# Performance work log

Hardware: AMD Instinct MI355X
Metric: run time of the kernel (lower is better)

The kernel has to match this reference:

```python
import jax, jax.numpy as jnp
import numpy as np

NEG = -1e30  # log-space 'minus infinity' that stays finite in fp32 arithmetic
BLANK = 0


def _lse3(a, b, c):
    m = jnp.maximum(jnp.maximum(a, b), c)
    return m + jnp.log(jnp.exp(a - m) + jnp.exp(b - m) + jnp.exp(c - m))


def setup_inputs() -> dict:
    key = jax.random.key(0)
    k1, k2, k3, k4 = jax.random.split(key, 4)
    B, T, C, L = 16, 512, 4096, 128
    scores = jax.random.normal(k1, (B, T, C), dtype=jnp.float32)
    labels = jax.random.randint(k2, (B, L), 1, C, dtype=jnp.int64)      # no blanks in targets
    feat_lens = jax.random.randint(k3, (B,), 384, T + 1, dtype=jnp.int64)
    label_lens = jax.random.randint(k4, (B,), 64, L + 1, dtype=jnp.int64)
    return {"scores": scores, "labels": labels, "feat_lens": feat_lens, "label_lens": label_lens}


def reference(scores, labels, feat_lens, label_lens):
    # scores: [B, T, C]. Matches torch: log_softmax then nn.CTCLoss(blank=0,
    # reduction='mean', zero_infinity=True).
    scores = scores.astype(jnp.float32)
    log_probs = jax.nn.log_softmax(scores, axis=-1)                      # [B, T, C]
    B, T, C = scores.shape
    L = labels.shape[1]
    S = 2 * L + 1  # extended label: blank, l1, blank, ..., lL, blank

    ext = jnp.full((B, S), BLANK, dtype=labels.dtype).at[:, 1::2].set(labels)
    # Gather per-(t, extended-symbol) log-probs once: [B, T, S]
    lp = jnp.take_along_axis(log_probs, jnp.broadcast_to(ext[:, None, :], (B, T, S)), axis=2)

    # skip transition s-2 -> s allowed iff ext[s] != blank and ext[s] != ext[s-2]
    skip = jnp.concatenate(
        [jnp.zeros((B, 2), bool), (ext[:, 2:] != ext[:, :-2]) & (ext[:, 2:] != BLANK)], axis=1)

    alpha0 = jnp.full((B, S), NEG, dtype=jnp.float32).at[:, 0].set(lp[:, 0, 0])
    alpha0 = alpha0.at[:, 1].set(jnp.where(label_lens > 0, lp[:, 0, 1], NEG))

    lp_t_first = jnp.swapaxes(lp, 0, 1)  # [T, B, S]

    def step(alpha, xs):
        lp_t, t = xs
        a1 = jnp.pad(alpha, ((0, 0), (1, 0)), constant_values=NEG)[:, :S]
        a2 = jnp.pad(alpha, ((0, 0), (2, 0)), constant_values=NEG)[:, :S]
        a2 = jnp.where(skip, a2, NEG)
        new = lp_t + _lse3(alpha, a1, a2)
        alpha = jnp.where((t < feat_lens)[:, None], new, alpha)  # freeze past feat_len
        return alpha, None

    alpha, _ = jax.lax.scan(step, alpha0, (lp_t_first[1:], jnp.arange(1, T)))

    end = 2 * label_lens  # index of final blank per sample
    a_end = jnp.take_along_axis(alpha, end[:, None], axis=1)[:, 0]
    a_end1 = jnp.where(
        label_lens > 0,
        jnp.take_along_axis(alpha, jnp.maximum(end - 1, 0)[:, None], axis=1)[:, 0], NEG)
    m = jnp.maximum(a_end, a_end1)
    log_lik = m + jnp.log(jnp.exp(a_end - m) + jnp.exp(a_end1 - m))
    loss = -log_lik
    loss = jnp.where(loss > 0.5e30, 0.0, loss)  # zero_infinity=True
    denom = jnp.maximum(label_lens, 1).astype(loss.dtype)
    return jnp.mean(loss / denom)  # torch 'mean': divide by target_lengths, then batch mean
```

## Files before the change

### kernel.cpp

```cpp
#include <hip/hip_runtime.h>

#define T_ 512
#define C_ 4096
#define L_ 128
#define NEGF (-1e30f)
#define RCPLN2 1.4426950408889634f
#define LN2 0.6931471805599453f

__device__ __forceinline__ float fexp2(float x) { return __builtin_amdgcn_exp2f(x); }
__device__ __forceinline__ float flog2(float x) { return __builtin_amdgcn_logf(x); }

__device__ __forceinline__ float lse2_2(float a, float b) {
  float m = fmaxf(a, b);
  float d = a - b;
  return m + flog2(1.0f + fexp2(-fabsf(d)));
}
__device__ __forceinline__ float lse3_2(float a, float b, float c) {
  float m = fmaxf(fmaxf(a, b), c);
  return m + flog2(fexp2(a - m) + fexp2(b - m) + fexp2(c - m));
}

__global__ __launch_bounds__(256) void k_lse_gather(
    const float* __restrict__ scores, const int* __restrict__ labels,
    const int* __restrict__ feat_lens,
    float* __restrict__ lp_lab, float* __restrict__ lp_blank) {
  const int row = blockIdx.x;
  const int b = row >> 9;
  const int t = row & (T_ - 1);
  if (t >= feat_lens[b]) return;

  __shared__ float sRow[C_];
  __shared__ float sSum[4];
  const float4* __restrict__ rp4 = (const float4*)(scores + (size_t)row * C_);
  float4* sRow4 = (float4*)sRow;
  const int tid = threadIdx.x;

  float s0 = 0.f, s1 = 0.f, s2 = 0.f, s3 = 0.f;
#pragma unroll
  for (int k = 0; k < 4; ++k) {
    float4 v = rp4[tid + 256 * k];
    sRow4[tid + 256 * k] = v;
    s0 += fexp2(v.x * RCPLN2);
    s1 += fexp2(v.y * RCPLN2);
    s2 += fexp2(v.z * RCPLN2);
    s3 += fexp2(v.w * RCPLN2);
  }
  float s = (s0 + s1) + (s2 + s3);
#pragma unroll
  for (int off = 32; off; off >>= 1) s += __shfl_down(s, off);
  const int wid = tid >> 6, lane = tid & 63;
  if (lane == 0) sSum[wid] = s;
  __syncthreads();
  const float l2sum = flog2((sSum[0] + sSum[1]) + (sSum[2] + sSum[3]));

  if (tid < L_) {
    const int lab = labels[b * L_ + tid];
    lp_lab[(size_t)row * L_ + tid] = sRow[lab] * RCPLN2 - l2sum;
  } else if (tid == L_) {
    lp_blank[row] = sRow[0] * RCPLN2 - l2sum;
  }
}

__global__ __launch_bounds__(128) void k_ctc_dp(
    const float* __restrict__ lp_lab, const float* __restrict__ lp_blank,
    const int* __restrict__ labels, const int* __restrict__ feat_lens,
    const int* __restrict__ label_lens, float* __restrict__ loss_out) {
  const int b = blockIdx.x;
  const int lane = threadIdx.x & 63;
  const int wid = threadIdx.x >> 6;
  const int flen = feat_lens[b];
  const int llen = label_lens[b];
  const int tm = flen >> 1;

  const int l0 = labels[b * L_ + 2 * lane];
  const int l1 = labels[b * L_ + 2 * lane + 1];
  const int lm1 = __shfl_up(l1, 1);
  const int ln0 = __shfl_down(l0, 1);
  const bool skip1 = (lane > 0) && (l0 != lm1);
  const bool skip3 = (l1 != l0);
  const bool skipd = (lane < 63) && (ln0 != l1);

  const float2* __restrict__ llp = (const float2*)(lp_lab + (size_t)b * T_ * L_);
  const float* __restrict__ lpl = lp_lab + (size_t)b * T_ * L_;
  const float* __restrict__ lbp = lp_blank + b * T_;

  __shared__ float sB[257];

  if (wid == 0) {
    const float2 ll0 = llp[lane];
    float a0 = (lane == 0) ? lbp[0] : NEGF;
    float a1 = (lane == 0) ? ll0.x : NEGF;
    float a2 = NEGF, a3 = NEGF, a4 = NEGF;
    float p = NEGF;

    float2 cc[4]; float cb[4];
#pragma unroll
    for (int k = 0; k < 4; ++k) {
      const int tt = min(1 + k, flen - 1);
      cc[k] = llp[tt * 64 + lane]; cb[k] = lbp[tt];
    }
    int t = 1;
    while (t <= tm) {
      float2 nc[4]; float nb[4];
#pragma unroll
      for (int k = 0; k < 4; ++k) {
        const int tt = min(t + 4 + k, flen - 1);
        nc[k] = llp[tt * 64 + lane]; nb[k] = lbp[tt];
      }
#pragma unroll
      for (int k = 0; k < 4; ++k) {
        if (t + k <= tm) {
          const float n3 = cc[k].y + lse3_2(a3, a2, skip3 ? a1 : NEGF);
          const float n4 = cb[k] + lse2_2(a4, a3);
          const float pn = __shfl_up(n3, 1);
          const float n0 = cb[k] + lse2_2(a0, p);
          const float n1 = cc[k].x + lse3_2(a1, a0, skip1 ? p : NEGF);
          const float n2 = cb[k] + lse2_2(a2, a1);
          a0 = n0; a1 = n1; a2 = n2; a3 = n3; a4 = n4;
          p = (lane == 0) ? NEGF : pn;
        }
      }
#pragma unroll
      for (int k = 0; k < 4; ++k) { cc[k] = nc[k]; cb[k] = nb[k]; }
      t += 4;
    }
    const float2 cce = llp[tm * 64 + lane];
    const float cbe = lbp[tm];
    const float c0 = a0 - cbe, c1 = a1 - cce.x, c2 = a2 - cbe, c3 = a3 - cce.y;
    const float c4 = a4 - cbe;
    __syncthreads();
    float v0 = c0 + sB[4 * lane + 0];
    float v1 = c1 + sB[4 * lane + 1];
    float v2 = c2 + sB[4 * lane + 2];
    float v3 = c3 + sB[4 * lane + 3];
    float m = fmaxf(fmaxf(v0, v1), fmaxf(v2, v3));
    float v4 = NEGF;
    if (lane == 63) { v4 = c4 + sB[256]; m = fmaxf(m, v4); }
#pragma unroll
    for (int off = 1; off < 64; off <<= 1) m = fmaxf(m, __shfl_xor(m, off));
    float sum = fexp2(v0 - m) + fexp2(v1 - m) + fexp2(v2 - m) + fexp2(v3 - m);
    if (lane == 63) sum += fexp2(v4 - m);
#pragma unroll
    for (int off = 1; off < 64; off <<= 1) sum += __shfl_xor(sum, off);
    if (lane == 0) {
      const float l2lik = m + flog2(sum);
      float loss = -LN2 * l2lik;
      if (loss > 0.5e30f) loss = 0.0f;
      loss_out[b] = loss / (float)llen;
    }
  } else {
    const int e = 2 * llen;
    const float ve = lbp[flen - 1];
    const float vo = lpl[(size_t)(flen - 1) * L_ + (llen - 1)];
    float b0 = (4 * lane == e) ? ve : NEGF;
    float b1 = (4 * lane + 1 == e - 1) ? vo : NEGF;
    float b2 = (4 * lane + 2 == e) ? ve : NEGF;
    float b3 = (4 * lane + 3 == e - 1) ? vo : NEGF;
    float b4 = (lane == 63 && e == 256) ? ve : NEGF;
    float q0 = __shfl_down(b0, 1); q0 = (lane == 63) ? b4 : q0;
    float q1 = __shfl_down(b1, 1); q1 = (lane == 63) ? NEGF : q1;

    float2 cc[4]; float cb[4];
    int t = flen - 2;
#pragma unroll
    for (int k = 0; k < 4; ++k) {
      const int tt = max(t - k, tm);
      cc[k] = llp[tt * 64 + lane]; cb[k] = lbp[tt];
    }
    while (t >= tm) {
      float2 nc[4]; float nb[4];
#pragma unroll
      for (int k = 0; k < 4; ++k) {
        const int tt = max(t - 4 - k, tm);
        nc[k] = llp[tt * 64 + lane]; nb[k] = lbp[tt];
      }
#pragma unroll
      for (int k = 0; k < 4; ++k) {
        if (t - k >= tm) {
          const float n0 = cb[k] + lse2_2(b0, b1);
          const float n1 = cc[k].x + lse3_2(b1, b2, skip3 ? b3 : NEGF);
          const float n4 = cb[k] + b4;
          const float q0n = __shfl_down(n0, 1);
          const float q1n = __shfl_down(n1, 1);
          const float n3 = cc[k].y + lse3_2(b3, q0, skipd ? q1 : NEGF);
          const float n2 = cb[k] + lse2_2(b2, b3);
          b0 = n0; b1 = n1; b2 = n2; b3 = n3; b4 = n4;
          q0 = (lane == 63) ? n4 : q0n;
          q1 = (lane == 63) ? NEGF : q1n;
        }
      }
#pragma unroll
      for (int k = 0; k < 4; ++k) { cc[k] = nc[k]; cb[k] = nb[k]; }
      t -= 4;
    }
    sB[4 * lane + 0] = b0;
    sB[4 * lane + 1] = b1;
    sB[4 * lane + 2] = b2;
    sB[4 * lane + 3] = b3;
    if (lane == 63) sB[256] = b4;
    __syncthreads();
  }
}

__global__ __launch_bounds__(64) void k_final(const float* __restrict__ loss_out,
                                              float* __restrict__ out, int B) {
  const int tid = threadIdx.x;
  float v = (tid < B) ? loss_out[tid] : 0.0f;
#pragma unroll
  for (int off = 32; off; off >>= 1) v += __shfl_down(v, off);
  if (tid == 0) out[0] = v / (float)B;
}

extern "C" void kernel_launch(void* const* d_in, const int* in_sizes, int n_in,
                              void* d_out, int out_size, void* d_ws, size_t ws_size,
                              hipStream_t stream) {
  const float* scores = (const float*)d_in[0];
  const int* labels = (const int*)d_in[1];
  const int* feat_lens = (const int*)d_in[2];
  const int* label_lens = (const int*)d_in[3];
  const int B = in_sizes[2];

  float* lp_lab = (float*)d_ws;
  float* lp_blank = lp_lab + (size_t)B * T_ * L_;
  float* loss_out = lp_blank + (size_t)B * T_;
  float* out = (float*)d_out;

  k_lse_gather<<<B * T_, 256, 0, stream>>>(scores, labels, feat_lens, lp_lab, lp_blank);
  k_ctc_dp<<<B, 128, 0, stream>>>(lp_lab, lp_blank, labels, feat_lens, label_lens, loss_out);
  k_final<<<1, 64, 0, stream>>>(loss_out, out, B);
}
```

Measured before the change: 231.8 us.

## Run CTC forward-backward recursion in scaled probability space instead of log space

The log-softmax gather now emits probabilities (exp2 of the log-prob), and the alpha/beta recursions switch from log-sum-exp to plain multiply-adds. Every two steps a wave-wide max rescales the state, and the log of that scale is accumulated so underflow is avoided. This removes the per-step exp/log transcendental chain on the serial DP critical path. In exchange it adds a wave-wide max reduction and a reciprocal every two steps, and precision changes, for example probabilities underflowing in fp32 when a single step's probabilities are very small.

Result: slower. 243.7 us (+5.1%).

```diff
diff --git a/kernel.cpp b/kernel.cpp
--- a/kernel.cpp
+++ b/kernel.cpp
@@ -3,27 +3,21 @@
 #define T_ 512
 #define C_ 4096
 #define L_ 128
-#define NEGF (-1e30f)
 #define RCPLN2 1.4426950408889634f
 #define LN2 0.6931471805599453f
+#define NEGL (-1e30f)
+#define SCALE_CTR 4.722366482869645e21f
+#define SCALE_LOG 72.0f
 
 __device__ __forceinline__ float fexp2(float x) { return __builtin_amdgcn_exp2f(x); }
 __device__ __forceinline__ float flog2(float x) { return __builtin_amdgcn_logf(x); }
-
-__device__ __forceinline__ float lse2_2(float a, float b) {
-  float m = fmaxf(a, b);
-  float d = a - b;
-  return m + flog2(1.0f + fexp2(-fabsf(d)));
-}
-__device__ __forceinline__ float lse3_2(float a, float b, float c) {
-  float m = fmaxf(fmaxf(a, b), c);
-  return m + flog2(fexp2(a - m) + fexp2(b - m) + fexp2(c - m));
-}
+__device__ __forceinline__ float frcp(float x)  { return __builtin_amdgcn_rcpf(x); }
+__device__ __forceinline__ float lg(float x)    { return (x > 0.f) ? flog2(x) : NEGL; }
 
 __global__ __launch_bounds__(256) void k_lse_gather(
     const float* __restrict__ scores, const int* __restrict__ labels,
     const int* __restrict__ feat_lens,
-    float* __restrict__ lp_lab, float* __restrict__ lp_blank) {
+    float* __restrict__ p_lab, float* __restrict__ p_blank) {
   const int row = blockIdx.x;
   const int b = row >> 9;
   const int t = row & (T_ - 1);
@@ -55,14 +49,14 @@
 
   if (tid < L_) {
     const int lab = labels[b * L_ + tid];
-    lp_lab[(size_t)row * L_ + tid] = sRow[lab] * RCPLN2 - l2sum;
+    p_lab[(size_t)row * L_ + tid] = fexp2(sRow[lab] * RCPLN2 - l2sum);
   } else if (tid == L_) {
-    lp_blank[row] = sRow[0] * RCPLN2 - l2sum;
+    p_blank[row] = fexp2(sRow[0] * RCPLN2 - l2sum);
   }
 }
 
 __global__ __launch_bounds__(128) void k_ctc_dp(
-    const float* __restrict__ lp_lab, const float* __restrict__ lp_blank,
+    const float* __restrict__ p_lab, const float* __restrict__ p_blank,
     const int* __restrict__ labels, const int* __restrict__ feat_lens,
     const int* __restrict__ label_lens, float* __restrict__ loss_out) {
   const int b = blockIdx.x;
@@ -80,18 +74,20 @@
   const bool skip3 = (l1 != l0);
   const bool skipd = (lane < 63) && (ln0 != l1);
 
-  const float2* __restrict__ llp = (const float2*)(lp_lab + (size_t)b * T_ * L_);
-  const float* __restrict__ lpl = lp_lab + (size_t)b * T_ * L_;
-  const float* __restrict__ lbp = lp_blank + b * T_;
+  const float2* __restrict__ llp = (const float2*)(p_lab + (size_t)b * T_ * L_);
+  const float* __restrict__ lpl = p_lab + (size_t)b * T_ * L_;
+  const float* __restrict__ lbp = p_blank + b * T_;
 
   __shared__ float sB[257];
+  __shared__ float sSb;
 
   if (wid == 0) {
     const float2 ll0 = llp[lane];
-    float a0 = (lane == 0) ? lbp[0] : NEGF;
-    float a1 = (lane == 0) ? ll0.x : NEGF;
-    float a2 = NEGF, a3 = NEGF, a4 = NEGF;
-    float p = NEGF;
+    float a0 = (lane == 0) ? lbp[0] : 0.f;
+    float a1 = (lane == 0) ? ll0.x : 0.f;
+    float a2 = 0.f, a3 = 0.f, a4 = 0.f;
+    float p = 0.f;
+    float Sa = 0.f;
 
     float2 cc[4]; float cb[4];
 #pragma unroll
@@ -110,14 +106,23 @@
 #pragma unroll
       for (int k = 0; k < 4; ++k) {
         if (t + k <= tm) {
-          const float n3 = cc[k].y + lse3_2(a3, a2, skip3 ? a1 : NEGF);
-          const float n4 = cb[k] + lse2_2(a4, a3);
+          const float n3 = cc[k].y * (a3 + a2 + (skip3 ? a1 : 0.f));
+          const float n4 = cb[k] * (a4 + a3);
           const float pn = __shfl_up(n3, 1);
-          const float n0 = cb[k] + lse2_2(a0, p);
-          const float n1 = cc[k].x + lse3_2(a1, a0, skip1 ? p : NEGF);
-          const float n2 = cb[k] + lse2_2(a2, a1);
-          a0 = n0; a1 = n1; a2 = n2; a3 = n3; a4 = n4;
-          p = (lane == 0) ? NEGF : pn;
+          const float n0 = cb[k] * (a0 + p);
+          const float n1 = cc[k].x * (a1 + a0 + (skip1 ? p : 0.f));
+          const float n2 = cb[k] * (a2 + a1);
+          a0 = n0; a1 = n1; a2 = n2; a3 = n3;
+          a4 = (lane == 63) ? n4 : 0.f;
+          p = (lane == 0) ? 0.f : pn;
+        }
+        if (k & 1) {
+          float m = fmaxf(fmaxf(fmaxf(a0, a1), fmaxf(a2, a3)), a4);
+#pragma unroll
+          for (int off = 1; off < 64; off <<= 1) m = fmaxf(m, __shfl_xor(m, off));
+          const float r = frcp(m) * SCALE_CTR;
+          Sa += flog2(m) - SCALE_LOG;
+          a0 *= r; a1 *= r; a2 *= r; a3 *= r; a4 *= r; p *= r;
         }
       }
 #pragma unroll
@@ -126,39 +131,41 @@
     }
     const float2 cce = llp[tm * 64 + lane];
     const float cbe = lbp[tm];
-    const float c0 = a0 - cbe, c1 = a1 - cce.x, c2 = a2 - cbe, c3 = a3 - cce.y;
-    const float c4 = a4 - cbe;
+    const float lb2 = flog2(cbe), lc0 = flog2(cce.x), lc1 = flog2(cce.y);
+    const float la0 = lg(a0), la1 = lg(a1), la2 = lg(a2), la3 = lg(a3);
+    const float la4 = lg(a4);
     __syncthreads();
-    float v0 = c0 + sB[4 * lane + 0];
-    float v1 = c1 + sB[4 * lane + 1];
-    float v2 = c2 + sB[4 * lane + 2];
-    float v3 = c3 + sB[4 * lane + 3];
-    float m = fmaxf(fmaxf(v0, v1), fmaxf(v2, v3));
-    float v4 = NEGF;
-    if (lane == 63) { v4 = c4 + sB[256]; m = fmaxf(m, v4); }
+    float w0 = la0 + sB[4 * lane + 0] - lb2;
+    float w1 = la1 + sB[4 * lane + 1] - lc0;
+    float w2 = la2 + sB[4 * lane + 2] - lb2;
+    float w3 = la3 + sB[4 * lane + 3] - lc1;
+    float m = fmaxf(fmaxf(w0, w1), fmaxf(w2, w3));
+    float w4 = NEGL;
+    if (lane == 63) { w4 = la4 + sB[256] - lb2; m = fmaxf(m, w4); }
 #pragma unroll
     for (int off = 1; off < 64; off <<= 1) m = fmaxf(m, __shfl_xor(m, off));
-    float sum = fexp2(v0 - m) + fexp2(v1 - m) + fexp2(v2 - m) + fexp2(v3 - m);
-    if (lane == 63) sum += fexp2(v4 - m);
+    float sum = fexp2(w0 - m) + fexp2(w1 - m) + fexp2(w2 - m) + fexp2(w3 - m);
+    if (lane == 63) sum += fexp2(w4 - m);
 #pragma unroll
     for (int off = 1; off < 64; off <<= 1) sum += __shfl_xor(sum, off);
     if (lane == 0) {
-      const float l2lik = m + flog2(sum);
+      const float l2lik = m + flog2(sum) + Sa + sSb;
       float loss = -LN2 * l2lik;
-      if (loss > 0.5e30f) loss = 0.0f;
+      if (loss > 0.5e30f || !(loss == loss)) loss = 0.0f;
       loss_out[b] = loss / (float)llen;
     }
   } else {
     const int e = 2 * llen;
     const float ve = lbp[flen - 1];
     const float vo = lpl[(size_t)(flen - 1) * L_ + (llen - 1)];
-    float b0 = (4 * lane == e) ? ve : NEGF;
-    float b1 = (4 * lane + 1 == e - 1) ? vo : NEGF;
-    float b2 = (4 * lane + 2 == e) ? ve : NEGF;
-    float b3 = (4 * lane + 3 == e - 1) ? vo : NEGF;
-    float b4 = (lane == 63 && e == 256) ? ve : NEGF;
+    float b0 = (4 * lane == e) ? ve : 0.f;
+    float b1 = (4 * lane + 1 == e - 1) ? vo : 0.f;
+    float b2 = (4 * lane + 2 == e) ? ve : 0.f;
+    float b3 = (4 * lane + 3 == e - 1) ? vo : 0.f;
+    float b4 = (lane == 63 && e == 256) ? ve : 0.f;
     float q0 = __shfl_down(b0, 1); q0 = (lane == 63) ? b4 : q0;
-    float q1 = __shfl_down(b1, 1); q1 = (lane == 63) ? NEGF : q1;
+    float q1 = __shfl_down(b1, 1); q1 = (lane == 63) ? 0.f : q1;
+    float Sb = 0.f;
 
     float2 cc[4]; float cb[4];
     int t = flen - 2;
@@ -177,27 +184,36 @@
 #pragma unroll
       for (int k = 0; k < 4; ++k) {
         if (t - k >= tm) {
-          const float n0 = cb[k] + lse2_2(b0, b1);
-          const float n1 = cc[k].x + lse3_2(b1, b2, skip3 ? b3 : NEGF);
-          const float n4 = cb[k] + b4;
+          const float n0 = cb[k] * (b0 + b1);
+          const float n1 = cc[k].x * (b1 + b2 + (skip3 ? b3 : 0.f));
+          const float n4 = cb[k] * b4;
           const float q0n = __shfl_down(n0, 1);
           const float q1n = __shfl_down(n1, 1);
-          const float n3 = cc[k].y + lse3_2(b3, q0, skipd ? q1 : NEGF);
-          const float n2 = cb[k] + lse2_2(b2, b3);
+          const float n3 = cc[k].y * (b3 + q0 + (skipd ? q1 : 0.f));
+          const float n2 = cb[k] * (b2 + b3);
           b0 = n0; b1 = n1; b2 = n2; b3 = n3; b4 = n4;
           q0 = (lane == 63) ? n4 : q0n;
-          q1 = (lane == 63) ? NEGF : q1n;
+          q1 = (lane == 63) ? 0.f : q1n;
+        }
+        if (k & 1) {
+          float m = fmaxf(fmaxf(fmaxf(b0, b1), fmaxf(b2, b3)), b4);
+#pragma unroll
+          for (int off = 1; off < 64; off <<= 1) m = fmaxf(m, __shfl_xor(m, off));
+          const float r = frcp(m) * SCALE_CTR;
+          Sb += flog2(m) - SCALE_LOG;
+          b0 *= r; b1 *= r; b2 *= r; b3 *= r; b4 *= r; q0 *= r; q1 *= r;
         }
       }
 #pragma unroll
       for (int k = 0; k < 4; ++k) { cc[k] = nc[k]; cb[k] = nb[k]; }
       t -= 4;
     }
-    sB[4 * lane + 0] = b0;
-    sB[4 * lane + 1] = b1;
-    sB[4 * lane + 2] = b2;
-    sB[4 * lane + 3] = b3;
-    if (lane == 63) sB[256] = b4;
+    sB[4 * lane + 0] = lg(b0);
+    sB[4 * lane + 1] = lg(b1);
+    sB[4 * lane + 2] = lg(b2);
+    sB[4 * lane + 3] = lg(b3);
+    if (lane == 63) sB[256] = lg(b4);
+    if (lane == 0) sSb = Sb;
     __syncthreads();
   }
 }
@@ -220,12 +236,12 @@
   const int* label_lens = (const int*)d_in[3];
   const int B = in_sizes[2];
 
-  float* lp_lab = (float*)d_ws;
-  float* lp_blank = lp_lab + (size_t)B * T_ * L_;
-  float* loss_out = lp_blank + (size_t)B * T_;
+  float* p_lab = (float*)d_ws;
+  float* p_blank = p_lab + (size_t)B * T_ * L_;
+  float* loss_out = p_blank + (size_t)B * T_;
   float* out = (float*)d_out;
 
-  k_lse_gather<<<B * T_, 256, 0, stream>>>(scores, labels, feat_lens, lp_lab, lp_blank);
-  k_ctc_dp<<<B, 128, 0, stream>>>(lp_lab, lp_blank, labels, feat_lens, label_lens, loss_out);
+  k_lse_gather<<<B * T_, 256, 0, stream>>>(scores, labels, feat_lens, p_lab, p_blank);
+  k_ctc_dp<<<B, 128, 0, stream>>>(p_lab, p_blank, labels, feat_lens, label_lens, loss_out);
   k_final<<<1, 64, 0, stream>>>(loss_out, out, B);
 }
```
